# Performance work log

Hardware: AMD Instinct MI355X
Metric: run time of the kernel (lower is better)

Reference implementation:

```python
import jax, jax.numpy as jnp
import numpy as np

MARGIN = 0.2
NEG_INF = -1e9  # safe stand-in for -inf when masking the max


def setup_inputs() -> dict:
    key = jax.random.key(0)
    k1, k2, k3 = jax.random.split(key, 3)
    B, D = 8192, 256
    p = jax.random.normal(k1, (B, D), dtype=jnp.float32)
    # module docstring says projections are normalized
    projections = p / jnp.linalg.norm(p, axis=1, keepdims=True)
    affordance_ids = jax.random.randint(k2, (B,), 0, 36, dtype=jnp.int64)
    instance_ids = jax.random.randint(k3, (B,), 0, 2048, dtype=jnp.int64)
    return {
        "projections": projections,
        "affordance_ids": affordance_ids,
        "instance_ids": instance_ids,
    }


def reference(projections, affordance_ids, instance_ids):
    # (B, B) cosine similarities
    sim = jnp.matmul(projections, projections.T)

    aff_eq = affordance_ids[:, None] == affordance_ids[None, :]
    inst_eq = instance_ids[:, None] == instance_ids[None, :]
    pos_mask = aff_eq & ~inst_eq          # same affordance, different instance
    neg_mask = ~aff_eq                    # different affordance

    # per-row hard negative: max similarity over negatives
    hard_neg = jnp.max(jnp.where(neg_mask, sim, NEG_INF), axis=1)  # (B,)

    # rows contribute only if they have >=1 positive AND >=1 negative
    valid_row = pos_mask.any(axis=1) & neg_mask.any(axis=1)        # (B,)
    pair_mask = pos_mask & valid_row[:, None]                      # (B, B)

    # margin loss for every (anchor i, positive j) pair
    losses = jnp.maximum(hard_neg[:, None] - sim + MARGIN, 0.0)

    total = jnp.sum(jnp.where(pair_mask, losses, 0.0))
    num_pairs = jnp.sum(pair_mask)
    return jnp.where(num_pairs > 0, total / num_pairs, 0.0)
```

## Files before the change

### kernel.cpp

```cpp
#include <hip/hip_runtime.h>

#define NB 8192
#define ND 256
#define NCLS 64
#define LOSS_MARGIN 0.2f
#define NEG_INF_F (-1e9f)
#define LMAXT 3
#define NBLK_LOSS (NCLS * LMAXT * LMAXT)
#define NTILE_T 2080
#define MAXCLS 640

typedef __attribute__((ext_vector_type(8))) __bf16 bf16x8;
typedef __attribute__((ext_vector_type(4))) float f32x4;

__device__ __forceinline__ unsigned short f2bf(float f) {
  unsigned u = __float_as_uint(f);
  unsigned r = (u + 0x7fffu + ((u >> 16) & 1u)) >> 16;
  return (unsigned short)r;
}

__device__ __forceinline__ void gl_lds16(const void* gsrc, void* ldst) {
  __builtin_amdgcn_global_load_lds(
      (const __attribute__((address_space(1))) void*)gsrc,
      (__attribute__((address_space(3))) void*)ldst, 16, 0, 0);
}

__global__ __launch_bounds__(1024) void prep_kernel(const float* __restrict__ P,
                                                    const int* __restrict__ aff,
                                                    const int* __restrict__ inst,
                                                    int* __restrict__ class_start,
                                                    unsigned short* __restrict__ Psort,
                                                    int* __restrict__ affSort,
                                                    int* __restrict__ instSort) {
  const int c = blockIdx.x;
  const int t = threadIdx.x;
  const int lane = t & 63, wave = t >> 6;
  __shared__ int wtot[16];
  __shared__ int s_off;
  __shared__ int lds_idx[MAXCLS];

  int lt = 0;
  for (int i = t; i < NB; i += 1024) lt += (aff[i] < c) ? 1 : 0;
  for (int off = 32; off; off >>= 1) lt += __shfl_down(lt, off);
  if (lane == 0) wtot[wave] = lt;
  __syncthreads();
  int base = 0;
  for (int w = 0; w < 16; ++w) base += wtot[w];
  if (t == 0) {
    class_start[c] = base;
    if (c == 0) class_start[NCLS] = NB;
  }
  __syncthreads();
  if (t == 0) s_off = 0;
  __syncthreads();

  for (int pass = 0; pass < NB / 1024; ++pass) {
    const int i = pass * 1024 + t;
    const bool m = (aff[i] == c);
    const unsigned long long mask = __ballot(m);
    if (lane == 0) wtot[wave] = __popcll(mask);
    __syncthreads();
    const int off = s_off;
    int prefix = 0;
    for (int w = 0; w < wave; ++w) prefix += wtot[w];
    if (m) {
      int pos = off + prefix + __popcll(mask & ((1ull << lane) - 1ull));
      if (pos < MAXCLS) lds_idx[pos] = i;
    }
    __syncthreads();
    if (t == 0) {
      int tot = 0;
      for (int w = 0; w < 16; ++w) tot += wtot[w];
      s_off = off + tot;
    }
    __syncthreads();
  }
  const int cnt = s_off;

  for (int k = wave; k < cnt; k += 16) {
    const int src = lds_idx[k];
    const int sr = base + k;
    const float4 v = ((const float4*)(P + (size_t)src * ND))[lane];
    ushort4 h;
    h.x = f2bf(v.x); h.y = f2bf(v.y); h.z = f2bf(v.z); h.w = f2bf(v.w);
    ((ushort4*)(Psort + (size_t)sr * ND))[lane] = h;
    if (lane == 0) {
      affSort[sr] = c;
      instSort[sr] = inst[src];
    }
  }
}

__global__ __launch_bounds__(256, 4) void simmax_mfma(const unsigned short* __restrict__ Psort,
                                                      const int* __restrict__ affSort,
                                                      float* __restrict__ part) {
  int wg = blockIdx.x;
  wg = (wg & 7) * (NTILE_T / 8) + (wg >> 3);
  int bi = (int)((129.0f - sqrtf(129.0f * 129.0f - 8.0f * (float)wg)) * 0.5f);
  while (bi * 64 - bi * (bi - 1) / 2 > wg) --bi;
  while ((bi + 1) * 64 - (bi + 1) * bi / 2 <= wg) ++bi;
  const int bj = bi + (wg - (bi * 64 - bi * (bi - 1) / 2));

  __shared__ __align__(16) unsigned short At[2][4096];
  __shared__ __align__(16) unsigned short Bt[2][4096];
  __shared__ int affI[128], affJ[128];
  __shared__ float rowmax_s[128][2];
  __shared__ float colmax_s[128][2];

  const int t = threadIdx.x;
  const int lane = t & 63;
  const int wave = t >> 6;
  const int r0 = bi * 128, c0 = bj * 128;

  const bool needMask = (affSort[c0] <= affSort[r0 + 127]);
  if (needMask) {
    if (t < 128) affI[t] = affSort[r0 + t];
    else affJ[t - 128] = affSort[c0 + (t - 128)];
  }

  const int wr = (wave >> 1) * 64;
  const int wc = (wave & 1) * 64;

  f32x4 acc[4][4];
#pragma unroll
  for (int m = 0; m < 4; ++m)
#pragma unroll
    for (int n = 0; n < 4; ++n) acc[m][n] = (f32x4){0.f, 0.f, 0.f, 0.f};

  const int ci0 = t, ci1 = 256 + t;
  const int kg0 = ci0 >> 7, rw0 = ci0 & 127;
  const int kg1 = ci1 >> 7, rw1 = ci1 & 127;

#define STAGE_SIM(B, KC)                                                      \
  do {                                                                        \
    gl_lds16(Psort + (size_t)(r0 + rw0) * ND + (KC) + kg0 * 8, &At[B][ci0 * 8]); \
    gl_lds16(Psort + (size_t)(c0 + rw0) * ND + (KC) + kg0 * 8, &Bt[B][ci0 * 8]); \
    gl_lds16(Psort + (size_t)(r0 + rw1) * ND + (KC) + kg1 * 8, &At[B][ci1 * 8]); \
    gl_lds16(Psort + (size_t)(c0 + rw1) * ND + (KC) + kg1 * 8, &Bt[B][ci1 * 8]); \
  } while (0)

  STAGE_SIM(0, 0);
  asm volatile("s_waitcnt vmcnt(0) lgkmcnt(0)" ::: "memory");
  __builtin_amdgcn_s_barrier();
  __builtin_amdgcn_sched_barrier(0);

  int cur = 0;
#pragma unroll 1
  for (int s = 0; s < 8; ++s) {
    if (s < 7) STAGE_SIM(cur ^ 1, (s + 1) * 32);
    const int kg = lane >> 4, lr = lane & 15;
    bf16x8 a[4], b[4];
#pragma unroll
    for (int m = 0; m < 4; ++m)
      a[m] = *(const bf16x8*)&At[cur][(kg * 128 + wr + m * 16 + lr) * 8];
#pragma unroll
    for (int n = 0; n < 4; ++n)
      b[n] = *(const bf16x8*)&Bt[cur][(kg * 128 + wc + n * 16 + lr) * 8];
#pragma unroll
    for (int m = 0; m < 4; ++m)
#pragma unroll
      for (int n = 0; n < 4; ++n)
        acc[m][n] = __builtin_amdgcn_mfma_f32_16x16x32_bf16(a[m], b[n], acc[m][n], 0, 0, 0);
    __builtin_amdgcn_sched_barrier(0);
    if (s < 7) {
      asm volatile("s_waitcnt vmcnt(0)" ::: "memory");
      __builtin_amdgcn_s_barrier();
      __builtin_amdgcn_sched_barrier(0);
    }
    cur ^= 1;
  }

  if (needMask) {
#pragma unroll
    for (int m = 0; m < 4; ++m) {
#pragma unroll
      for (int r = 0; r < 4; ++r) {
        const int lrow = wr + m * 16 + (lane >> 4) * 4 + r;
        const int ai = affI[lrow];
        float rmax = NEG_INF_F;
#pragma unroll
        for (int n = 0; n < 4; ++n) {
          const int lcol = wc + n * 16 + (lane & 15);
          if (affJ[lcol] != ai) rmax = fmaxf(rmax, acc[m][n][r]);
        }
        rmax = fmaxf(rmax, __shfl_xor(rmax, 1));
        rmax = fmaxf(rmax, __shfl_xor(rmax, 2));
        rmax = fmaxf(rmax, __shfl_xor(rmax, 4));
        rmax = fmaxf(rmax, __shfl_xor(rmax, 8));
        if ((lane & 15) == 0) rowmax_s[lrow][wc >> 6] = rmax;
      }
    }
    if (bi != bj) {
#pragma unroll
      for (int n = 0; n < 4; ++n) {
        const int lcol = wc + n * 16 + (lane & 15);
        const int aj = affJ[lcol];
        float cmax = NEG_INF_F;
#pragma unroll
        for (int m = 0; m < 4; ++m) {
          const int lrb = wr + m * 16 + (lane >> 4) * 4;
#pragma unroll
          for (int r = 0; r < 4; ++r)
            if (affI[lrb + r] != aj) cmax = fmaxf(cmax, acc[m][n][r]);
        }
        cmax = fmaxf(cmax, __shfl_xor(cmax, 16));
        cmax = fmaxf(cmax, __shfl_xor(cmax, 32));
        if (lane < 16) colmax_s[lcol][wr >> 6] = cmax;
      }
    }
  } else {
#pragma unroll
    for (int m = 0; m < 4; ++m) {
#pragma unroll
      for (int r = 0; r < 4; ++r) {
        float rmax = fmaxf(fmaxf(acc[m][0][r], acc[m][1][r]),
                           fmaxf(acc[m][2][r], acc[m][3][r]));
        rmax = fmaxf(rmax, __shfl_xor(rmax, 1));
        rmax = fmaxf(rmax, __shfl_xor(rmax, 2));
        rmax = fmaxf(rmax, __shfl_xor(rmax, 4));
        rmax = fmaxf(rmax, __shfl_xor(rmax, 8));
        if ((lane & 15) == 0)
          rowmax_s[wr + m * 16 + (lane >> 4) * 4 + r][wc >> 6] = rmax;
      }
    }
#pragma unroll
    for (int n = 0; n < 4; ++n) {
      float cmax = NEG_INF_F;
#pragma unroll
      for (int m = 0; m < 4; ++m)
#pragma unroll
        for (int r = 0; r < 4; ++r) cmax = fmaxf(cmax, acc[m][n][r]);
      cmax = fmaxf(cmax, __shfl_xor(cmax, 16));
      cmax = fmaxf(cmax, __shfl_xor(cmax, 32));
      if (lane < 16) colmax_s[wc + n * 16 + (lane & 15)][wr >> 6] = cmax;
    }
  }
  __syncthreads();
  if (t < 128) {
    part[(size_t)bj * NB + (r0 + t)] = fmaxf(rowmax_s[t][0], rowmax_s[t][1]);
  } else if (bi != bj) {
    const int cc = t - 128;
    part[(size_t)bi * NB + (c0 + cc)] = fmaxf(colmax_s[cc][0], colmax_s[cc][1]);
  }
#undef STAGE_SIM
}

__global__ __launch_bounds__(256, 4) void loss_mfma(const unsigned short* __restrict__ Psort,
                                                    const int* __restrict__ class_start,
                                                    const int* __restrict__ instSort,
                                                    const float* __restrict__ part,
                                                    float* __restrict__ bsum,
                                                    int* __restrict__ bcnt) {
  const int c = blockIdx.z;
  const int ti = blockIdx.x, tj = blockIdx.y;
  const int bid = (c * LMAXT + ti) * LMAXT + tj;
  const int t = threadIdx.x;
  const int base = class_start[c];
  const int cnt = class_start[c + 1] - base;
  const int nt = (cnt + 127) >> 7;
  if (ti >= nt || tj >= nt || cnt >= NB) {
    if (t == 0) { bsum[bid] = 0.f; bcnt[bid] = 0; }
    return;
  }

  __shared__ __align__(16) unsigned short At[2][4096];
  __shared__ __align__(16) unsigned short Bt[2][4096];
  __shared__ int instI[128], instJ[128];
  __shared__ float hnI[128];

  const int lane = t & 63;
  const int wave = t >> 6;

  if (t < 128) {
    int ri = ti * 128 + t;
    int gi = base + (ri < cnt ? ri : 0);
    instI[t] = instSort[gi];
    float m = NEG_INF_F;
#pragma unroll 16
    for (int q = 0; q < 64; ++q) m = fmaxf(m, part[(size_t)q * NB + gi]);
    hnI[t] = m;
  } else {
    int tt = t - 128;
    int rj = tj * 128 + tt;
    int gj = base + (rj < cnt ? rj : 0);
    instJ[tt] = instSort[gj];
  }

  const int wr = (wave >> 1) * 64;
  const int wc = (wave & 1) * 64;

  f32x4 acc[4][4];
#pragma unroll
  for (int m = 0; m < 4; ++m)
#pragma unroll
    for (int n = 0; n < 4; ++n) acc[m][n] = (f32x4){0.f, 0.f, 0.f, 0.f};

  const int ci0 = t, ci1 = 256 + t;
  const int kg0 = ci0 >> 7, rw0 = ci0 & 127;
  const int kg1 = ci1 >> 7, rw1 = ci1 & 127;
  const int ra0 = base + (ti * 128 + rw0 < cnt ? ti * 128 + rw0 : 0);
  const int ra1 = base + (ti * 128 + rw1 < cnt ? ti * 128 + rw1 : 0);
  const int rb0 = base + (tj * 128 + rw0 < cnt ? tj * 128 + rw0 : 0);
  const int rb1 = base + (tj * 128 + rw1 < cnt ? tj * 128 + rw1 : 0);

#define STAGE_LOSS(B, KC)                                               \
  do {                                                                  \
    gl_lds16(Psort + (size_t)ra0 * ND + (KC) + kg0 * 8, &At[B][ci0 * 8]); \
    gl_lds16(Psort + (size_t)rb0 * ND + (KC) + kg0 * 8, &Bt[B][ci0 * 8]); \
    gl_lds16(Psort + (size_t)ra1 * ND + (KC) + kg1 * 8, &At[B][ci1 * 8]); \
    gl_lds16(Psort + (size_t)rb1 * ND + (KC) + kg1 * 8, &Bt[B][ci1 * 8]); \
  } while (0)

  STAGE_LOSS(0, 0);
  asm volatile("s_waitcnt vmcnt(0) lgkmcnt(0)" ::: "memory");
  __builtin_amdgcn_s_barrier();
  __builtin_amdgcn_sched_barrier(0);

  int cur = 0;
#pragma unroll 1
  for (int s = 0; s < 8; ++s) {
    if (s < 7) STAGE_LOSS(cur ^ 1, (s + 1) * 32);
    const int kg = lane >> 4, lr = lane & 15;
    bf16x8 a[4], b[4];
#pragma unroll
    for (int m = 0; m < 4; ++m)
      a[m] = *(const bf16x8*)&At[cur][(kg * 128 + wr + m * 16 + lr) * 8];
#pragma unroll
    for (int n = 0; n < 4; ++n)
      b[n] = *(const bf16x8*)&Bt[cur][(kg * 128 + wc + n * 16 + lr) * 8];
#pragma unroll
    for (int m = 0; m < 4; ++m)
#pragma unroll
      for (int n = 0; n < 4; ++n)
        acc[m][n] = __builtin_amdgcn_mfma_f32_16x16x32_bf16(a[m], b[n], acc[m][n], 0, 0, 0);
    __builtin_amdgcn_sched_barrier(0);
    if (s < 7) {
      asm volatile("s_waitcnt vmcnt(0)" ::: "memory");
      __builtin_amdgcn_s_barrier();
      __builtin_amdgcn_sched_barrier(0);
    }
    cur ^= 1;
  }

  float lsum = 0.f;
  int lcnt = 0;
#pragma unroll
  for (int m = 0; m < 4; ++m) {
#pragma unroll
    for (int r = 0; r < 4; ++r) {
      const int lrow = wr + m * 16 + (lane >> 4) * 4 + r;
      const int ri = ti * 128 + lrow;
      if (ri >= cnt) continue;
      const float hnv = hnI[lrow];
      const int ii = instI[lrow];
#pragma unroll
      for (int n = 0; n < 4; ++n) {
        const int lcol = wc + n * 16 + (lane & 15);
        const int rj = tj * 128 + lcol;
        if (rj < cnt && instJ[lcol] != ii) {
          lsum += fmaxf(hnv - acc[m][n][r] + LOSS_MARGIN, 0.f);
          lcnt += 1;
        }
      }
    }
  }

  for (int off = 32; off; off >>= 1) {
    lsum += __shfl_down(lsum, off);
    lcnt += __shfl_down(lcnt, off);
  }
  __shared__ float wsum[4];
  __shared__ int wcnt[4];
  if (lane == 0) { wsum[wave] = lsum; wcnt[wave] = lcnt; }
  __syncthreads();
  if (t == 0) {
    bsum[bid] = wsum[0] + wsum[1] + wsum[2] + wsum[3];
    bcnt[bid] = wcnt[0] + wcnt[1] + wcnt[2] + wcnt[3];
  }
#undef STAGE_LOSS
}

__global__ __launch_bounds__(256) void finalize_kernel(const float* __restrict__ bsum,
                                                       const int* __restrict__ bcnt,
                                                       float* __restrict__ out) {
  const int t = threadIdx.x;
  float s = 0.f;
  int n = 0;
  for (int i = t; i < NBLK_LOSS; i += 256) { s += bsum[i]; n += bcnt[i]; }
  for (int off = 32; off; off >>= 1) {
    s += __shfl_down(s, off);
    n += __shfl_down(n, off);
  }
  __shared__ float wsum[4];
  __shared__ int wcnt[4];
  if ((t & 63) == 0) { wsum[t >> 6] = s; wcnt[t >> 6] = n; }
  __syncthreads();
  if (t == 0) {
    const float S = wsum[0] + wsum[1] + wsum[2] + wsum[3];
    const int N = wcnt[0] + wcnt[1] + wcnt[2] + wcnt[3];
    out[0] = (N > 0) ? (S / (float)N) : 0.0f;
  }
}

extern "C" void kernel_launch(void* const* d_in, const int* in_sizes, int n_in,
                              void* d_out, int out_size, void* d_ws, size_t ws_size,
                              hipStream_t stream) {
  const float* P = (const float*)d_in[0];
  const int* aff = (const int*)d_in[1];
  const int* inst = (const int*)d_in[2];
  float* out = (float*)d_out;

  unsigned short* Psort = (unsigned short*)d_ws;
  float* part = (float*)((char*)d_ws + (size_t)NB * ND * 2);
  int* ibase = (int*)((char*)part + (size_t)64 * NB * 4);
  int* class_start = ibase;
  int* affSort     = ibase + NCLS + 1;
  int* instSort    = ibase + NCLS + 1 + NB;
  float* bsum = (float*)(ibase + NCLS + 1 + 2 * NB);
  int* bcnt   = ibase + NCLS + 1 + 2 * NB + NBLK_LOSS;

  prep_kernel<<<NCLS, 1024, 0, stream>>>(P, aff, inst, class_start, Psort,
                                         affSort, instSort);
  simmax_mfma<<<NTILE_T, 256, 0, stream>>>(Psort, affSort, part);
  loss_mfma<<<dim3(LMAXT, LMAXT, NCLS), 256, 0, stream>>>(Psort, class_start, instSort,
                                                          part, bsum, bcnt);
  finalize_kernel<<<1, 256, 0, stream>>>(bsum, bcnt, out);
}
```

Measured before the change: 99.11 us.

## Split prep into index build and parallel gather-convert; shrink simmax LDS footprint

The per-class prep kernel, which had only 64 blocks doing both index building and the bf16 gather, is split in two. One kernel writes class-sorted indices to global memory. A second kernel, launched with many more blocks, gathers and converts the rows. In simmax, the A/B buffers and the reduction scratch now share one LDS array, the affinity label caches in LDS are dropped in favour of direct global reads, and launch bounds rise to 5 blocks per CU for more occupancy. The cost is an extra kernel launch and global reads of affSort in the mask epilogue.

```diff
diff --git a/kernel.cpp b/kernel.cpp
--- a/kernel.cpp
+++ b/kernel.cpp
@@ -8,7 +8,6 @@
 #define LMAXT 3
 #define NBLK_LOSS (NCLS * LMAXT * LMAXT)
 #define NTILE_T 2080
-#define MAXCLS 640
 
 typedef __attribute__((ext_vector_type(8))) __bf16 bf16x8;
 typedef __attribute__((ext_vector_type(4))) float f32x4;
@@ -25,19 +24,14 @@
       (__attribute__((address_space(3))) void*)ldst, 16, 0, 0);
 }
 
-__global__ __launch_bounds__(1024) void prep_kernel(const float* __restrict__ P,
-                                                    const int* __restrict__ aff,
-                                                    const int* __restrict__ inst,
-                                                    int* __restrict__ class_start,
-                                                    unsigned short* __restrict__ Psort,
-                                                    int* __restrict__ affSort,
-                                                    int* __restrict__ instSort) {
+__global__ __launch_bounds__(1024) void build_idx_fused(const int* __restrict__ aff,
+                                                        int* __restrict__ class_start,
+                                                        int* __restrict__ class_idx) {
   const int c = blockIdx.x;
   const int t = threadIdx.x;
   const int lane = t & 63, wave = t >> 6;
   __shared__ int wtot[16];
   __shared__ int s_off;
-  __shared__ int lds_idx[MAXCLS];
 
   int lt = 0;
   for (int i = t; i < NB; i += 1024) lt += (aff[i] < c) ? 1 : 0;
@@ -63,10 +57,9 @@
     const int off = s_off;
     int prefix = 0;
     for (int w = 0; w < wave; ++w) prefix += wtot[w];
-    if (m) {
-      int pos = off + prefix + __popcll(mask & ((1ull << lane) - 1ull));
-      if (pos < MAXCLS) lds_idx[pos] = i;
-    }
+    if (m)
+      class_idx[base + off + prefix +
+                __popcll(mask & ((1ull << lane) - 1ull))] = i;
     __syncthreads();
     if (t == 0) {
       int tot = 0;
@@ -75,23 +68,35 @@
     }
     __syncthreads();
   }
-  const int cnt = s_off;
-
-  for (int k = wave; k < cnt; k += 16) {
-    const int src = lds_idx[k];
-    const int sr = base + k;
-    const float4 v = ((const float4*)(P + (size_t)src * ND))[lane];
+}
+
+__global__ __launch_bounds__(256) void gather_convert(const float* __restrict__ P,
+                                                      const int* __restrict__ aff,
+                                                      const int* __restrict__ inst,
+                                                      const int* __restrict__ class_idx,
+                                                      unsigned short* __restrict__ Psort,
+                                                      int* __restrict__ affSort,
+                                                      int* __restrict__ instSort) {
+  const int t = threadIdx.x;
+  const int sr = blockIdx.x * 8 + (t >> 5);
+  const int c = t & 31;
+  const int src = class_idx[sr];
+  const float4* ps = (const float4*)(P + (size_t)src * ND);
+  ushort4* pd = (ushort4*)(Psort + (size_t)sr * ND);
+#pragma unroll
+  for (int q = 0; q < 2; ++q) {
+    float4 v = ps[c + q * 32];
     ushort4 h;
     h.x = f2bf(v.x); h.y = f2bf(v.y); h.z = f2bf(v.z); h.w = f2bf(v.w);
-    ((ushort4*)(Psort + (size_t)sr * ND))[lane] = h;
-    if (lane == 0) {
-      affSort[sr] = c;
-      instSort[sr] = inst[src];
-    }
-  }
-}
-
-__global__ __launch_bounds__(256, 4) void simmax_mfma(const unsigned short* __restrict__ Psort,
+    pd[c + q * 32] = h;
+  }
+  if (c == 0) {
+    affSort[sr] = aff[src];
+    instSort[sr] = inst[src];
+  }
+}
+
+__global__ __launch_bounds__(256, 5) void simmax_mfma(const unsigned short* __restrict__ Psort,
                                                       const int* __restrict__ affSort,
                                                       float* __restrict__ part) {
   int wg = blockIdx.x;
@@ -101,11 +106,9 @@
   while ((bi + 1) * 64 - (bi + 1) * bi / 2 <= wg) ++bi;
   const int bj = bi + (wg - (bi * 64 - bi * (bi - 1) / 2));
 
-  __shared__ __align__(16) unsigned short At[2][4096];
-  __shared__ __align__(16) unsigned short Bt[2][4096];
-  __shared__ int affI[128], affJ[128];
-  __shared__ float rowmax_s[128][2];
-  __shared__ float colmax_s[128][2];
+  __shared__ __align__(16) unsigned short smemu[16384];
+  float* rowmax_s = (float*)&smemu[0];
+  float* colmax_s = (float*)&smemu[512];
 
   const int t = threadIdx.x;
   const int lane = t & 63;
@@ -113,10 +116,6 @@
   const int r0 = bi * 128, c0 = bj * 128;
 
   const bool needMask = (affSort[c0] <= affSort[r0 + 127]);
-  if (needMask) {
-    if (t < 128) affI[t] = affSort[r0 + t];
-    else affJ[t - 128] = affSort[c0 + (t - 128)];
-  }
 
   const int wr = (wave >> 1) * 64;
   const int wc = (wave & 1) * 64;
@@ -133,10 +132,14 @@
 
 #define STAGE_SIM(B, KC)                                                      \
   do {                                                                        \
-    gl_lds16(Psort + (size_t)(r0 + rw0) * ND + (KC) + kg0 * 8, &At[B][ci0 * 8]); \
-    gl_lds16(Psort + (size_t)(c0 + rw0) * ND + (KC) + kg0 * 8, &Bt[B][ci0 * 8]); \
-    gl_lds16(Psort + (size_t)(r0 + rw1) * ND + (KC) + kg1 * 8, &At[B][ci1 * 8]); \
-    gl_lds16(Psort + (size_t)(c0 + rw1) * ND + (KC) + kg1 * 8, &Bt[B][ci1 * 8]); \
+    gl_lds16(Psort + (size_t)(r0 + rw0) * ND + (KC) + kg0 * 8,                \
+             &smemu[(B) * 4096 + ci0 * 8]);                                   \
+    gl_lds16(Psort + (size_t)(c0 + rw0) * ND + (KC) + kg0 * 8,                \
+             &smemu[8192 + (B) * 4096 + ci0 * 8]);                            \
+    gl_lds16(Psort + (size_t)(r0 + rw1) * ND + (KC) + kg1 * 8,                \
+             &smemu[(B) * 4096 + ci1 * 8]);                                   \
+    gl_lds16(Psort + (size_t)(c0 + rw1) * ND + (KC) + kg1 * 8,                \
+             &smemu[8192 + (B) * 4096 + ci1 * 8]);                            \
   } while (0)
 
   STAGE_SIM(0, 0);
@@ -152,10 +155,10 @@
     bf16x8 a[4], b[4];
 #pragma unroll
     for (int m = 0; m < 4; ++m)
-      a[m] = *(const bf16x8*)&At[cur][(kg * 128 + wr + m * 16 + lr) * 8];
+      a[m] = *(const bf16x8*)&smemu[cur * 4096 + (kg * 128 + wr + m * 16 + lr) * 8];
 #pragma unroll
     for (int n = 0; n < 4; ++n)
-      b[n] = *(const bf16x8*)&Bt[cur][(kg * 128 + wc + n * 16 + lr) * 8];
+      b[n] = *(const bf16x8*)&smemu[8192 + cur * 4096 + (kg * 128 + wc + n * 16 + lr) * 8];
 #pragma unroll
     for (int m = 0; m < 4; ++m)
 #pragma unroll
@@ -176,36 +179,36 @@
 #pragma unroll
       for (int r = 0; r < 4; ++r) {
         const int lrow = wr + m * 16 + (lane >> 4) * 4 + r;
-        const int ai = affI[lrow];
+        const int ai = affSort[r0 + lrow];
         float rmax = NEG_INF_F;
 #pragma unroll
         for (int n = 0; n < 4; ++n) {
           const int lcol = wc + n * 16 + (lane & 15);
-          if (affJ[lcol] != ai) rmax = fmaxf(rmax, acc[m][n][r]);
+          if (affSort[c0 + lcol] != ai) rmax = fmaxf(rmax, acc[m][n][r]);
         }
         rmax = fmaxf(rmax, __shfl_xor(rmax, 1));
         rmax = fmaxf(rmax, __shfl_xor(rmax, 2));
         rmax = fmaxf(rmax, __shfl_xor(rmax, 4));
         rmax = fmaxf(rmax, __shfl_xor(rmax, 8));
-        if ((lane & 15) == 0) rowmax_s[lrow][wc >> 6] = rmax;
+        if ((lane & 15) == 0) rowmax_s[lrow * 2 + (wc >> 6)] = rmax;
       }
     }
     if (bi != bj) {
 #pragma unroll
       for (int n = 0; n < 4; ++n) {
         const int lcol = wc + n * 16 + (lane & 15);
-        const int aj = affJ[lcol];
+        const int aj = affSort[c0 + lcol];
         float cmax = NEG_INF_F;
 #pragma unroll
         for (int m = 0; m < 4; ++m) {
           const int lrb = wr + m * 16 + (lane >> 4) * 4;
 #pragma unroll
           for (int r = 0; r < 4; ++r)
-            if (affI[lrb + r] != aj) cmax = fmaxf(cmax, acc[m][n][r]);
+            if (affSort[r0 + lrb + r] != aj) cmax = fmaxf(cmax, acc[m][n][r]);
         }
         cmax = fmaxf(cmax, __shfl_xor(cmax, 16));
         cmax = fmaxf(cmax, __shfl_xor(cmax, 32));
-        if (lane < 16) colmax_s[lcol][wr >> 6] = cmax;
+        if (lane < 16) colmax_s[lcol * 2 + (wr >> 6)] = cmax;
       }
     }
   } else {
@@ -220,7 +223,7 @@
         rmax = fmaxf(rmax, __shfl_xor(rmax, 4));
         rmax = fmaxf(rmax, __shfl_xor(rmax, 8));
         if ((lane & 15) == 0)
-          rowmax_s[wr + m * 16 + (lane >> 4) * 4 + r][wc >> 6] = rmax;
+          rowmax_s[(wr + m * 16 + (lane >> 4) * 4 + r) * 2 + (wc >> 6)] = rmax;
       }
     }
 #pragma unroll
@@ -232,15 +235,15 @@
         for (int r = 0; r < 4; ++r) cmax = fmaxf(cmax, acc[m][n][r]);
       cmax = fmaxf(cmax, __shfl_xor(cmax, 16));
       cmax = fmaxf(cmax, __shfl_xor(cmax, 32));
-      if (lane < 16) colmax_s[wc + n * 16 + (lane & 15)][wr >> 6] = cmax;
+      if (lane < 16) colmax_s[(wc + n * 16 + (lane & 15)) * 2 + (wr >> 6)] = cmax;
     }
   }
   __syncthreads();
   if (t < 128) {
-    part[(size_t)bj * NB + (r0 + t)] = fmaxf(rowmax_s[t][0], rowmax_s[t][1]);
+    part[(size_t)bj * NB + (r0 + t)] = fmaxf(rowmax_s[t * 2], rowmax_s[t * 2 + 1]);
   } else if (bi != bj) {
     const int cc = t - 128;
-    part[(size_t)bi * NB + (c0 + cc)] = fmaxf(colmax_s[cc][0], colmax_s[cc][1]);
+    part[(size_t)bi * NB + (c0 + cc)] = fmaxf(colmax_s[cc * 2], colmax_s[cc * 2 + 1]);
   }
 #undef STAGE_SIM
 }
@@ -414,13 +417,15 @@
   float* part = (float*)((char*)d_ws + (size_t)NB * ND * 2);
   int* ibase = (int*)((char*)part + (size_t)64 * NB * 4);
   int* class_start = ibase;
-  int* affSort     = ibase + NCLS + 1;
-  int* instSort    = ibase + NCLS + 1 + NB;
-  float* bsum = (float*)(ibase + NCLS + 1 + 2 * NB);
-  int* bcnt   = ibase + NCLS + 1 + 2 * NB + NBLK_LOSS;
-
-  prep_kernel<<<NCLS, 1024, 0, stream>>>(P, aff, inst, class_start, Psort,
-                                         affSort, instSort);
+  int* class_idx   = ibase + NCLS + 1;
+  int* affSort     = ibase + NCLS + 1 + NB;
+  int* instSort    = ibase + NCLS + 1 + 2 * NB;
+  float* bsum = (float*)(ibase + NCLS + 1 + 3 * NB);
+  int* bcnt   = ibase + NCLS + 1 + 3 * NB + NBLK_LOSS;
+
+  build_idx_fused<<<NCLS, 1024, 0, stream>>>(aff, class_start, class_idx);
+  gather_convert<<<NB / 8, 256, 0, stream>>>(P, aff, inst, class_idx, Psort,
+                                             affSort, instSort);
   simmax_mfma<<<NTILE_T, 256, 0, stream>>>(Psort, affSort, part);
   loss_mfma<<<dim3(LMAXT, LMAXT, NCLS), 256, 0, stream>>>(Psort, class_start, instSort,
                                                           part, bsum, bcnt);
```

Result: slower. 134.1 us (+35.3%).
